# Performance work log

Hardware: AMD Instinct MI355X
Metric: run time of the kernel (lower is better)

## Reference

```python
import jax, jax.numpy as jnp
import numpy as np

NOISE_STD = 0.1
NUM_EXPERTS = 32
TOPK = 2
OUTPUT_DIM = 256


def setup_inputs() -> dict:
    key = jax.random.key(0)
    k_x, k_n, k_gw, k_ew = jax.random.split(key, 4)
    N, D_IN = 32768, 256
    E, D_OUT = NUM_EXPERTS, OUTPUT_DIM
    x = jax.random.normal(k_x, (N, D_IN), dtype=jnp.float32)
    noise = jax.random.normal(k_n, (N, E), dtype=jnp.float32)
    # gate: nn.Linear(input_dim, num_experts) default init scale
    gate_w = jax.random.normal(k_gw, (E, D_IN), dtype=jnp.float32) / jnp.sqrt(D_IN).astype(jnp.float32)
    gate_b = jnp.zeros((E,), dtype=jnp.float32)
    # experts: nn.Linear(input_dim, output_dim * num_experts), xavier_uniform weight, zero bias
    lim = float(np.sqrt(6.0 / (D_IN + D_OUT * E)))
    experts_w = jax.random.uniform(k_ew, (D_OUT * E, D_IN), minval=-lim, maxval=lim, dtype=jnp.float32)
    experts_b = jnp.zeros((D_OUT * E,), dtype=jnp.float32)
    return {"x": x, "noise": noise, "gate_w": gate_w, "gate_b": gate_b,
            "experts_w": experts_w, "experts_b": experts_b}


def reference(x, noise, gate_w, gate_b, experts_w, experts_b):
    N = x.shape[0]
    E, D = NUM_EXPERTS, OUTPUT_DIM
    # gating with noisy logits
    gate_logits = x @ gate_w.T + gate_b + noise * NOISE_STD          # [N, E]
    gate_probs = jax.nn.softmax(gate_logits, axis=-1)                # [N, E]
    # load-balance auxiliary loss
    gate_probs_mean = gate_probs.mean(axis=0)                        # [E]
    expected = 1.0 / E
    load_balance_loss = jnp.mean((gate_probs_mean - expected) ** 2) * E
    # top-k routing
    topk_probs, topk_idx = jax.lax.top_k(gate_probs, TOPK)           # [N, k]
    # all-expert dense linear, then gather the selected experts
    expert_outputs = (x @ experts_w.T + experts_b).reshape(N, E, D)  # [N, E, D]
    sel = jnp.take_along_axis(expert_outputs, topk_idx[:, :, None], axis=1)  # [N, k, D]
    output = jnp.einsum('bk,bkd->bd', topk_probs, sel)               # [N, D]
    return output, load_balance_loss
```

## Files before the change

kernel.cpp:

```cpp
#include <hip/hip_runtime.h>
#include <hip/hip_bf16.h>

#define N_ROWS 32768
#define D_INP  256
#define NEXP   32
#define D_OUTP 256

typedef __attribute__((ext_vector_type(4))) float f32x4;
typedef __attribute__((ext_vector_type(8))) short bf16x8;

__device__ inline unsigned short f2b(float f) {
    union { __hip_bfloat16 h; unsigned short u; } cv;
    cv.h = __float2bfloat16(f);
    return cv.u;
}

__global__ __launch_bounds__(256) void gate_kernel(
    const float* __restrict__ x, const float* __restrict__ noise,
    const float* __restrict__ gw, const float* __restrict__ gb,
    unsigned short* __restrict__ xb, float* __restrict__ tkp,
    int* __restrict__ tki, float* __restrict__ esum, int* __restrict__ ecnt)
{
    __shared__ float gws[NEXP * 260];
    __shared__ float xs[128 * 132];
    __shared__ float lsum[NEXP];
    __shared__ int   lcnt[NEXP];

    int tid = threadIdx.x;
    int row0 = blockIdx.x * 128;

    #pragma unroll
    for (int it = 0; it < 8; ++it) {
        int q = it * 256 + tid;
        int e = q >> 6;
        int k = (q & 63) * 4;
        float4 v = ((const float4*)gw)[q];
        *(float4*)&gws[e * 260 + k] = v;
    }
    if (tid < NEXP) { lsum[tid] = 0.f; lcnt[tid] = 0; }

    int e4 = tid & 7;
    int rq = tid >> 3;

    float acc[4][4];
    #pragma unroll
    for (int m = 0; m < 4; m++)
        #pragma unroll
        for (int n = 0; n < 4; n++) acc[m][n] = 0.f;

    for (int h = 0; h < 2; ++h) {
        int ko = h * 128;
        __syncthreads();
        #pragma unroll
        for (int it = 0; it < 16; ++it) {
            int idx = it * 256 + tid;
            int r = idx >> 5;
            int f = idx & 31;
            float4 v = *(const float4*)(x + (size_t)(row0 + r) * D_INP + ko + f * 4);
            *(float4*)&xs[r * 132 + f * 4] = v;
            unsigned short b[4] = { f2b(v.x), f2b(v.y), f2b(v.z), f2b(v.w) };
            *(ushort4*)(xb + (size_t)(row0 + r) * D_INP + ko + f * 4) = *(ushort4*)b;
        }
        __syncthreads();
        #pragma unroll 4
        for (int c = 0; c < 32; ++c) {
            float4 xv[4], wv[4];
            #pragma unroll
            for (int m = 0; m < 4; m++)
                xv[m] = *(float4*)&xs[(rq + 32 * m) * 132 + c * 4];
            #pragma unroll
            for (int n = 0; n < 4; n++)
                wv[n] = *(float4*)&gws[(e4 + 8 * n) * 260 + ko + c * 4];
            #pragma unroll
            for (int m = 0; m < 4; m++)
                #pragma unroll
                for (int n = 0; n < 4; n++)
                    acc[m][n] = fmaf(xv[m].x, wv[n].x,
                                fmaf(xv[m].y, wv[n].y,
                                fmaf(xv[m].z, wv[n].z,
                                fmaf(xv[m].w, wv[n].w, acc[m][n]))));
        }
    }

    #pragma unroll
    for (int m = 0; m < 4; m++) {
        int R = row0 + rq + 32 * m;
        float l[4], p[4];
        #pragma unroll
        for (int n = 0; n < 4; n++) {
            int E = e4 + 8 * n;
            l[n] = acc[m][n] + gb[E] + 0.1f * noise[(size_t)R * NEXP + E];
        }
        float mx = fmaxf(fmaxf(l[0], l[1]), fmaxf(l[2], l[3]));
        #pragma unroll
        for (int s = 1; s < 8; s <<= 1) mx = fmaxf(mx, __shfl_xor(mx, s));
        float sum = 0.f;
        #pragma unroll
        for (int n = 0; n < 4; n++) { p[n] = expf(l[n] - mx); sum += p[n]; }
        #pragma unroll
        for (int s = 1; s < 8; s <<= 1) sum += __shfl_xor(sum, s);
        float inv = 1.f / sum;
        #pragma unroll
        for (int n = 0; n < 4; n++) p[n] *= inv;

        float bp = p[0]; int bi = e4;
        #pragma unroll
        for (int n = 1; n < 4; n++) if (p[n] > bp) { bp = p[n]; bi = e4 + 8 * n; }
        #pragma unroll
        for (int s = 1; s < 8; s <<= 1) {
            float op = __shfl_xor(bp, s); int oi = __shfl_xor(bi, s);
            if (op > bp || (op == bp && oi < bi)) { bp = op; bi = oi; }
        }
        float bp2 = -1.f; int bi2 = 0;
        #pragma unroll
        for (int n = 0; n < 4; n++) {
            int E = e4 + 8 * n;
            float q = (E == bi) ? -1.f : p[n];
            if (q > bp2 || (q == bp2 && E < bi2)) { bp2 = q; bi2 = E; }
        }
        #pragma unroll
        for (int s = 1; s < 8; s <<= 1) {
            float op = __shfl_xor(bp2, s); int oi = __shfl_xor(bi2, s);
            if (op > bp2 || (op == bp2 && oi < bi2)) { bp2 = op; bi2 = oi; }
        }
        if (e4 == 0) {
            tkp[R * 2] = bp;  tkp[R * 2 + 1] = bp2;
            tki[R * 2] = bi;  tki[R * 2 + 1] = bi2;
            atomicAdd(&lcnt[bi], 1); atomicAdd(&lcnt[bi2], 1);
        }
        #pragma unroll
        for (int n = 0; n < 4; n++) atomicAdd(&lsum[e4 + 8 * n], p[n]);
    }
    __syncthreads();
    if (tid < NEXP) {
        unsafeAtomicAdd(&esum[tid], lsum[tid]);
        atomicAdd(&ecnt[tid], lcnt[tid]);
    }
}

__global__ __launch_bounds__(256) void cast_w_kernel(
    const float* __restrict__ w, unsigned short* __restrict__ wb)
{
    size_t i = (size_t)blockIdx.x * 256 + threadIdx.x;
    float4 v = ((const float4*)w)[i];
    unsigned short t[4] = { f2b(v.x), f2b(v.y), f2b(v.z), f2b(v.w) };
    ((ushort4*)wb)[i] = *(ushort4*)t;
}

__global__ void scan_kernel(const float* __restrict__ esum, const int* __restrict__ ecnt,
                            int* __restrict__ offs, int* __restrict__ cursor,
                            int* __restrict__ toff, float* __restrict__ loss_out)
{
    int t = threadIdx.x;
    if (t == 0) {
        int acc = 0, ta = 0;
        for (int e = 0; e < NEXP; e++) {
            offs[e] = acc; cursor[e] = acc; toff[e] = ta;
            int c = ecnt[e];
            acc += c; ta += (c + 63) >> 6;
        }
        offs[NEXP] = acc; toff[NEXP] = ta;
    }
    if (t < 32) {
        float d = esum[t] * (1.f / N_ROWS) - (1.f / NEXP);
        float v = d * d;
        #pragma unroll
        for (int s = 16; s > 0; s >>= 1) v += __shfl_xor(v, s, 32);
        if (t == 0) *loss_out = v;
    }
}

__global__ __launch_bounds__(256) void build_list_kernel(
    const int* __restrict__ tki, int* __restrict__ cursor, int* __restrict__ list)
{
    __shared__ int lcnt[NEXP], lbase[NEXP];
    int tid = threadIdx.x;
    if (tid < NEXP) lcnt[tid] = 0;
    __syncthreads();
    int r = blockIdx.x * 256 + tid;
    int e0 = tki[r * 2], e1 = tki[r * 2 + 1];
    int p0 = atomicAdd(&lcnt[e0], 1);
    int p1 = atomicAdd(&lcnt[e1], 1);
    __syncthreads();
    if (tid < NEXP) lbase[tid] = atomicAdd(&cursor[tid], lcnt[tid]);
    __syncthreads();
    list[lbase[e0] + p0] = r * 2;
    list[lbase[e1] + p1] = r * 2 + 1;
}

__global__ __launch_bounds__(256) void moe_gemm_kernel(
    const unsigned short* __restrict__ xb, const unsigned short* __restrict__ wb,
    const float* __restrict__ expb, const float* __restrict__ tkp,
    const int* __restrict__ list, const int* __restrict__ offs,
    const int* __restrict__ toff, float* __restrict__ out, float* __restrict__ y1)
{
    int nblk = toff[NEXP];
    int b = blockIdx.x;
    if (b >= nblk) return;
    int e = 0;
    while (toff[e + 1] <= b) e++;
    int tile = b - toff[e];
    int m0 = offs[e] + tile * 64;
    int cnt = offs[e + 1] - offs[e];
    int nrows = min(64, cnt - tile * 64);

    __shared__ unsigned short xa[64 * 256];
    __shared__ int   srow[64];
    __shared__ int   sslot[64];
    __shared__ float sprob[64];
    int tid = threadIdx.x;
    if (tid < 64) {
        if (tid < nrows) {
            int ent = list[m0 + tid];
            srow[tid]  = ent >> 1;
            sslot[tid] = ent & 1;
            sprob[tid] = tkp[ent];
        } else { srow[tid] = -1; sslot[tid] = 0; sprob[tid] = 0.f; }
    }
    __syncthreads();

    {
        int r_ = tid >> 2;
        int gr = srow[r_];
        const uint4* src = (const uint4*)(xb + (size_t)(gr < 0 ? 0 : gr) * D_INP);
        uint4* dst = (uint4*)xa;
        int swz = r_ & 7;
        #pragma unroll
        for (int i = 0; i < 8; ++i) {
            int c = (tid & 3) + 4 * i;
            dst[r_ * 32 + (c ^ swz)] = src[c];
        }
    }
    __syncthreads();

    int wave = tid >> 6;
    int lane = tid & 63;
    int lr = lane & 15;
    int kg = lane >> 4;
    int n0 = wave * 64;
    int aswz = lr & 7;

    f32x4 acc[4][4];
    #pragma unroll
    for (int mm = 0; mm < 4; mm++)
        #pragma unroll
        for (int nn = 0; nn < 4; nn++)
            acc[mm][nn] = (f32x4){0.f, 0.f, 0.f, 0.f};

    for (int kk = 0; kk < 8; kk++) {
        int chunk = kk * 4 + kg;
        int aoff = (chunk ^ aswz) * 8;
        bf16x8 a[4], bb[4];
        #pragma unroll
        for (int mm = 0; mm < 4; mm++)
            a[mm] = *(const bf16x8*)&xa[(mm * 16 + lr) * 256 + aoff];
        #pragma unroll
        for (int nn = 0; nn < 4; nn++)
            bb[nn] = *(const bf16x8*)(wb + ((size_t)e * 256 + n0 + nn * 16 + lr) * D_INP + kk * 32 + kg * 8);
        #pragma unroll
        for (int mm = 0; mm < 4; mm++)
            #pragma unroll
            for (int nn = 0; nn < 4; nn++)
                acc[mm][nn] = __builtin_amdgcn_mfma_f32_16x16x32_bf16(a[mm], bb[nn], acc[mm][nn], 0, 0, 0);
    }

    #pragma unroll
    for (int mm = 0; mm < 4; mm++) {
        #pragma unroll
        for (int j = 0; j < 4; j++) {
            int lrow = mm * 16 + kg * 4 + j;
            int rr = srow[lrow];
            if (rr >= 0) {
                float pp = sprob[lrow];
                float* dst = sslot[lrow] ? y1 : out;
                #pragma unroll
                for (int nn = 0; nn < 4; nn++) {
                    int col = n0 + nn * 16 + lr;
                    dst[(size_t)rr * D_OUTP + col] = (acc[mm][nn][j] + expb[e * 256 + col]) * pp;
                }
            }
        }
    }
}

__global__ __launch_bounds__(256) void combine_kernel(
    const float* __restrict__ y1, float* __restrict__ out)
{
    size_t i = ((size_t)blockIdx.x * 256 + threadIdx.x) * 4;
    float4 a = *(const float4*)(out + i);
    float4 b = *(const float4*)(y1 + i);
    a.x += b.x; a.y += b.y; a.z += b.z; a.w += b.w;
    *(float4*)(out + i) = a;
}

extern "C" void kernel_launch(void* const* d_in, const int* in_sizes, int n_in,
                              void* d_out, int out_size, void* d_ws, size_t ws_size,
                              hipStream_t stream)
{
    const float* x   = (const float*)d_in[0];
    const float* noi = (const float*)d_in[1];
    const float* gw  = (const float*)d_in[2];
    const float* gb  = (const float*)d_in[3];
    const float* ew  = (const float*)d_in[4];
    const float* eb  = (const float*)d_in[5];
    float* out = (float*)d_out;

    char* p = (char*)d_ws;
    unsigned short* xb = (unsigned short*)p; p += (size_t)N_ROWS * D_INP * 2;
    unsigned short* wb = (unsigned short*)p; p += (size_t)NEXP * D_OUTP * D_INP * 2;
    float* y1   = (float*)p; p += (size_t)N_ROWS * D_OUTP * 4;
    float* tkp  = (float*)p; p += (size_t)N_ROWS * 2 * 4;
    int*   tki  = (int*)p;   p += (size_t)N_ROWS * 2 * 4;
    int*   list = (int*)p;   p += (size_t)N_ROWS * 2 * 4;
    float* esum = (float*)p; p += 32 * 4;
    int*   ecnt = (int*)p;   p += 32 * 4;
    int*   offs = (int*)p;   p += 33 * 4;
    int*   curs = (int*)p;   p += 33 * 4;
    int*   toff = (int*)p;   p += 33 * 4;

    hipMemsetAsync(esum, 0, 64 * 4, stream);

    gate_kernel<<<N_ROWS / 128, 256, 0, stream>>>(x, noi, gw, gb, xb, tkp, tki, esum, ecnt);
    cast_w_kernel<<<(NEXP * D_OUTP * D_INP / 4) / 256, 256, 0, stream>>>(ew, wb);
    scan_kernel<<<1, 64, 0, stream>>>(esum, ecnt, offs, curs, toff, out + (size_t)N_ROWS * D_OUTP);
    build_list_kernel<<<N_ROWS / 256, 256, 0, stream>>>(tki, curs, list);
    moe_gemm_kernel<<<(N_ROWS * 2 / 64) + NEXP, 256, 0, stream>>>(xb, wb, eb, tkp, list, offs, toff, out, y1);
    combine_kernel<<<N_ROWS * D_OUTP / 4 / 256, 256, 0, stream>>>(y1, out);
}
```

Measured before the change: 180.2 us.

## Fuse weight cast into gate, precompute tile table, bf16 intermediates, 32-row tiles

Moves the expert-weight fp32-to-bf16 cast into the gate kernel, which removes one launch. The scan becomes a parallel warp prefix sum that also writes a per-tile table, so GEMM blocks stop searching linearly for their expert. GEMM tiles shrink to 32 rows, and the block index is interleaved across experts. Each tile's output is staged through LDS and written as coalesced bf16 rows into two buffers, and the combine kernel adds them in fp32. This cuts intermediate memory traffic and improves write coalescing, but the bf16 intermediates lose precision and the smaller tiles reuse each weight load less.

Result: no change. 179.1 us (-0.6%).

```diff
diff --git a/kernel.cpp b/kernel.cpp
--- a/kernel.cpp
+++ b/kernel.cpp
@@ -5,6 +5,8 @@
 #define D_INP  256
 #define NEXP   32
 #define D_OUTP 256
+#define TROWS  32
+#define NTILES 2080
 
 typedef __attribute__((ext_vector_type(4))) float f32x4;
 typedef __attribute__((ext_vector_type(8))) short bf16x8;
@@ -14,10 +16,14 @@
     cv.h = __float2bfloat16(f);
     return cv.u;
 }
+__device__ inline float b2f(unsigned short u) {
+    union { unsigned v; float f; } c; c.v = ((unsigned)u) << 16; return c.f;
+}
 
 __global__ __launch_bounds__(256) void gate_kernel(
     const float* __restrict__ x, const float* __restrict__ noise,
     const float* __restrict__ gw, const float* __restrict__ gb,
+    const float* __restrict__ ew, unsigned short* __restrict__ wbh,
     unsigned short* __restrict__ xb, float* __restrict__ tkp,
     int* __restrict__ tki, float* __restrict__ esum, int* __restrict__ ecnt)
 {
@@ -131,6 +137,18 @@
         #pragma unroll
         for (int n = 0; n < 4; n++) atomicAdd(&lsum[e4 + 8 * n], p[n]);
     }
+
+    {
+        size_t base = (size_t)blockIdx.x * 2048;
+        #pragma unroll
+        for (int it = 0; it < 8; ++it) {
+            size_t q = base + it * 256 + tid;
+            float4 v = ((const float4*)ew)[q];
+            unsigned short t4[4] = { f2b(v.x), f2b(v.y), f2b(v.z), f2b(v.w) };
+            ((ushort4*)wbh)[q] = *(ushort4*)t4;
+        }
+    }
+
     __syncthreads();
     if (tid < NEXP) {
         unsafeAtomicAdd(&esum[tid], lsum[tid]);
@@ -138,35 +156,49 @@
     }
 }
 
-__global__ __launch_bounds__(256) void cast_w_kernel(
-    const float* __restrict__ w, unsigned short* __restrict__ wb)
-{
-    size_t i = (size_t)blockIdx.x * 256 + threadIdx.x;
-    float4 v = ((const float4*)w)[i];
-    unsigned short t[4] = { f2b(v.x), f2b(v.y), f2b(v.z), f2b(v.w) };
-    ((ushort4*)wb)[i] = *(ushort4*)t;
-}
-
-__global__ void scan_kernel(const float* __restrict__ esum, const int* __restrict__ ecnt,
-                            int* __restrict__ offs, int* __restrict__ cursor,
-                            int* __restrict__ toff, float* __restrict__ loss_out)
-{
+__global__ __launch_bounds__(256) void scan_kernel(
+    const float* __restrict__ esum, const int* __restrict__ ecnt,
+    int* __restrict__ offs, int* __restrict__ cursor,
+    int* __restrict__ tile_tab, float* __restrict__ loss_out)
+{
+    __shared__ int s_offs[NEXP + 1], s_toff[NEXP + 1];
     int t = threadIdx.x;
-    if (t == 0) {
-        int acc = 0, ta = 0;
-        for (int e = 0; e < NEXP; e++) {
-            offs[e] = acc; cursor[e] = acc; toff[e] = ta;
-            int c = ecnt[e];
-            acc += c; ta += (c + 63) >> 6;
-        }
-        offs[NEXP] = acc; toff[NEXP] = ta;
-    }
     if (t < 32) {
+        int c = ecnt[t];
+        int ic = c, itc = (c + TROWS - 1) / TROWS;
+        #pragma unroll
+        for (int s = 1; s < 32; s <<= 1) {
+            int a = __shfl_up(ic, s, 32);  if (t >= s) ic += a;
+            int b = __shfl_up(itc, s, 32); if (t >= s) itc += b;
+        }
+        s_offs[t + 1] = ic; s_toff[t + 1] = itc;
+        if (t == 0) { s_offs[0] = 0; s_toff[0] = 0; }
+    }
+    __syncthreads();
+    if (t < 32) {
+        offs[t] = s_offs[t]; cursor[t] = s_offs[t];
+        if (t == 0) offs[NEXP] = s_offs[NEXP];
         float d = esum[t] * (1.f / N_ROWS) - (1.f / NEXP);
         float v = d * d;
         #pragma unroll
         for (int s = 16; s > 0; s >>= 1) v += __shfl_xor(v, s, 32);
         if (t == 0) *loss_out = v;
+    }
+    int ntile = s_toff[NEXP];
+    for (int b = t; b < NTILES; b += 256) {
+        if (b < ntile) {
+            int e = 0;
+            #pragma unroll
+            for (int s = 16; s; s >>= 1)
+                if (e + s <= 31 && s_toff[e + s] <= b) e += s;
+            int tile = b - s_toff[e];
+            int m0 = s_offs[e] + tile * TROWS;
+            int nr = min(TROWS, s_offs[e + 1] - m0);
+            tile_tab[b * 2]     = e | (nr << 8);
+            tile_tab[b * 2 + 1] = m0;
+        } else {
+            tile_tab[b * 2] = 0; tile_tab[b * 2 + 1] = 0;
+        }
     }
 }
 
@@ -191,26 +223,22 @@
 __global__ __launch_bounds__(256) void moe_gemm_kernel(
     const unsigned short* __restrict__ xb, const unsigned short* __restrict__ wb,
     const float* __restrict__ expb, const float* __restrict__ tkp,
-    const int* __restrict__ list, const int* __restrict__ offs,
-    const int* __restrict__ toff, float* __restrict__ out, float* __restrict__ y1)
-{
-    int nblk = toff[NEXP];
-    int b = blockIdx.x;
-    if (b >= nblk) return;
-    int e = 0;
-    while (toff[e + 1] <= b) e++;
-    int tile = b - toff[e];
-    int m0 = offs[e] + tile * 64;
-    int cnt = offs[e + 1] - offs[e];
-    int nrows = min(64, cnt - tile * 64);
-
-    __shared__ unsigned short xa[64 * 256];
-    __shared__ int   srow[64];
-    __shared__ int   sslot[64];
-    __shared__ float sprob[64];
+    const int* __restrict__ list, const int* __restrict__ tile_tab,
+    unsigned short* __restrict__ y0, unsigned short* __restrict__ y1)
+{
+    int b = (blockIdx.x & 7) * (NTILES / 8) + (blockIdx.x >> 3);
+    int hdr = tile_tab[b * 2];
+    int e = hdr & 0xff, nr = hdr >> 8;
+    if (nr == 0) return;
+    int m0 = tile_tab[b * 2 + 1];
+
+    __shared__ unsigned short xa[TROWS * 256];
+    __shared__ int   srow[TROWS];
+    __shared__ int   sslot[TROWS];
+    __shared__ float sprob[TROWS];
     int tid = threadIdx.x;
-    if (tid < 64) {
-        if (tid < nrows) {
+    if (tid < TROWS) {
+        if (tid < nr) {
             int ent = list[m0 + tid];
             srow[tid]  = ent >> 1;
             sslot[tid] = ent & 1;
@@ -220,14 +248,14 @@
     __syncthreads();
 
     {
-        int r_ = tid >> 2;
-        int gr = srow[r_];
-        const uint4* src = (const uint4*)(xb + (size_t)(gr < 0 ? 0 : gr) * D_INP);
+        int r_ = tid >> 3;
+        int gr = srow[r_]; if (gr < 0) gr = 0;
+        const uint4* src = (const uint4*)(xb + (size_t)gr * D_INP);
         uint4* dst = (uint4*)xa;
         int swz = r_ & 7;
         #pragma unroll
-        for (int i = 0; i < 8; ++i) {
-            int c = (tid & 3) + 4 * i;
+        for (int i = 0; i < 4; ++i) {
+            int c = (tid & 7) + 8 * i;
             dst[r_ * 32 + (c ^ swz)] = src[c];
         }
     }
@@ -240,57 +268,88 @@
     int n0 = wave * 64;
     int aswz = lr & 7;
 
-    f32x4 acc[4][4];
-    #pragma unroll
-    for (int mm = 0; mm < 4; mm++)
+    f32x4 acc[2][4];
+    #pragma unroll
+    for (int mm = 0; mm < 2; mm++)
         #pragma unroll
         for (int nn = 0; nn < 4; nn++)
             acc[mm][nn] = (f32x4){0.f, 0.f, 0.f, 0.f};
 
+    #pragma unroll
     for (int kk = 0; kk < 8; kk++) {
         int chunk = kk * 4 + kg;
         int aoff = (chunk ^ aswz) * 8;
-        bf16x8 a[4], bb[4];
-        #pragma unroll
-        for (int mm = 0; mm < 4; mm++)
+        bf16x8 a[2], bb[4];
+        #pragma unroll
+        for (int mm = 0; mm < 2; mm++)
             a[mm] = *(const bf16x8*)&xa[(mm * 16 + lr) * 256 + aoff];
         #pragma unroll
         for (int nn = 0; nn < 4; nn++)
             bb[nn] = *(const bf16x8*)(wb + ((size_t)e * 256 + n0 + nn * 16 + lr) * D_INP + kk * 32 + kg * 8);
         #pragma unroll
-        for (int mm = 0; mm < 4; mm++)
+        for (int mm = 0; mm < 2; mm++)
             #pragma unroll
             for (int nn = 0; nn < 4; nn++)
                 acc[mm][nn] = __builtin_amdgcn_mfma_f32_16x16x32_bf16(a[mm], bb[nn], acc[mm][nn], 0, 0, 0);
     }
-
-    #pragma unroll
-    for (int mm = 0; mm < 4; mm++) {
-        #pragma unroll
-        for (int j = 0; j < 4; j++) {
-            int lrow = mm * 16 + kg * 4 + j;
-            int rr = srow[lrow];
-            if (rr >= 0) {
+    __syncthreads();
+
+    {
+        float bias[4];
+        #pragma unroll
+        for (int nn = 0; nn < 4; nn++) bias[nn] = expb[e * 256 + n0 + nn * 16 + lr];
+        #pragma unroll
+        for (int mm = 0; mm < 2; mm++) {
+            #pragma unroll
+            for (int j = 0; j < 4; j++) {
+                int lrow = mm * 16 + kg * 4 + j;
                 float pp = sprob[lrow];
-                float* dst = sslot[lrow] ? y1 : out;
                 #pragma unroll
                 for (int nn = 0; nn < 4; nn++) {
-                    int col = n0 + nn * 16 + lr;
-                    dst[(size_t)rr * D_OUTP + col] = (acc[mm][nn][j] + expb[e * 256 + col]) * pp;
+                    float v = (acc[mm][nn][j] + bias[nn]) * pp;
+                    xa[lrow * 256 + n0 + nn * 16 + lr] = f2b(v);
                 }
             }
         }
     }
+    __syncthreads();
+
+    {
+        int r_ = tid >> 3;
+        int gr = srow[r_];
+        if (gr >= 0) {
+            unsigned short* dstb = (sslot[r_] ? y1 : y0) + (size_t)gr * D_OUTP;
+            const uint4* src = (const uint4*)(xa + r_ * 256);
+            uint4* dst = (uint4*)dstb;
+            #pragma unroll
+            for (int i = 0; i < 4; ++i) {
+                int c = (tid & 7) + 8 * i;
+                dst[c] = src[c];
+            }
+        }
+    }
 }
 
 __global__ __launch_bounds__(256) void combine_kernel(
-    const float* __restrict__ y1, float* __restrict__ out)
-{
-    size_t i = ((size_t)blockIdx.x * 256 + threadIdx.x) * 4;
-    float4 a = *(const float4*)(out + i);
-    float4 b = *(const float4*)(y1 + i);
-    a.x += b.x; a.y += b.y; a.z += b.z; a.w += b.w;
-    *(float4*)(out + i) = a;
+    const unsigned short* __restrict__ y0, const unsigned short* __restrict__ y1,
+    float* __restrict__ out)
+{
+    size_t i = ((size_t)blockIdx.x * 256 + threadIdx.x) * 8;
+    uint4 a = *(const uint4*)(y0 + i);
+    uint4 b = *(const uint4*)(y1 + i);
+    const unsigned short* ap = (const unsigned short*)&a;
+    const unsigned short* bp = (const unsigned short*)&b;
+    float4 o0, o1;
+    o0.x = b2f(ap[0]) + b2f(bp[0]);
+    o0.y = b2f(ap[1]) + b2f(bp[1]);
+    o0.z = b2f(ap[2]) + b2f(bp[2]);
+    o0.w = b2f(ap[3]) + b2f(bp[3]);
+    o1.x = b2f(ap[4]) + b2f(bp[4]);
+    o1.y = b2f(ap[5]) + b2f(bp[5]);
+    o1.z = b2f(ap[6]) + b2f(bp[6]);
+    o1.w = b2f(ap[7]) + b2f(bp[7]);
+    *(float4*)(out + i)     = o0;
+    *(float4*)(out + i + 4) = o1;
 }
 
 extern "C" void kernel_launch(void* const* d_in, const int* in_sizes, int n_in,
@@ -308,22 +367,22 @@
     char* p = (char*)d_ws;
     unsigned short* xb = (unsigned short*)p; p += (size_t)N_ROWS * D_INP * 2;
     unsigned short* wb = (unsigned short*)p; p += (size_t)NEXP * D_OUTP * D_INP * 2;
-    float* y1   = (float*)p; p += (size_t)N_ROWS * D_OUTP * 4;
+    unsigned short* y0 = (unsigned short*)p; p += (size_t)N_ROWS * D_OUTP * 2;
+    unsigned short* y1 = (unsigned short*)p; p += (size_t)N_ROWS * D_OUTP * 2;
     float* tkp  = (float*)p; p += (size_t)N_ROWS * 2 * 4;
     int*   tki  = (int*)p;   p += (size_t)N_ROWS * 2 * 4;
     int*   list = (int*)p;   p += (size_t)N_ROWS * 2 * 4;
+    int*   ttab = (int*)p;   p += (size_t)NTILES * 2 * 4;
     float* esum = (float*)p; p += 32 * 4;
     int*   ecnt = (int*)p;   p += 32 * 4;
     int*   offs = (int*)p;   p += 33 * 4;
     int*   curs = (int*)p;   p += 33 * 4;
-    int*   toff = (int*)p;   p += 33 * 4;
 
     hipMemsetAsync(esum, 0, 64 * 4, stream);
 
-    gate_kernel<<<N_ROWS / 128, 256, 0, stream>>>(x, noi, gw, gb, xb, tkp, tki, esum, ecnt);
-    cast_w_kernel<<<(NEXP * D_OUTP * D_INP / 4) / 256, 256, 0, stream>>>(ew, wb);
-    scan_kernel<<<1, 64, 0, stream>>>(esum, ecnt, offs, curs, toff, out + (size_t)N_ROWS * D_OUTP);
+    gate_kernel<<<N_ROWS / 128, 256, 0, stream>>>(x, noi, gw, gb, ew, wb, xb, tkp, tki, esum, ecnt);
+    scan_kernel<<<1, 256, 0, stream>>>(esum, ecnt, offs, curs, ttab, out + (size_t)N_ROWS * D_OUTP);
     build_list_kernel<<<N_ROWS / 256, 256, 0, stream>>>(tki, curs, list);
-    moe_gemm_kernel<<<(N_ROWS * 2 / 64) + NEXP, 256, 0, stream>>>(xb, wb, eb, tkp, list, offs, toff, out, y1);
-    combine_kernel<<<N_ROWS * D_OUTP / 4 / 256, 256, 0, stream>>>(y1, out);
-}
+    moe_gemm_kernel<<<NTILES, 256, 0, stream>>>(xb, wb, eb, tkp, list, ttab, y0, y1);
+    combine_kernel<<<N_ROWS * D_OUTP / 8 / 256, 256, 0, stream>>>(y0, y1, out);
+}
```
